# Kernel tuning notes

Hardware: AMD Instinct MI355X
Metric: run time of the kernel (lower is better)

## Reference

```python
import jax, jax.numpy as jnp
import numpy as np

B, E, H, SEQ = 4096, 512, 512, 128


def setup_inputs() -> dict:
    key = jax.random.key(0)
    ks = jax.random.split(key, 7)
    s = 1.0 / np.sqrt(H)  # PyTorch LSTM init scale
    return {
        "start_emb": jax.random.normal(ks[0], (B, 1, E), dtype=jnp.float32),
        "h0": jax.random.normal(ks[1], (1, B, H), dtype=jnp.float32),
        "c0": jax.random.normal(ks[2], (1, B, H), dtype=jnp.float32),
        "w_ih": jax.random.normal(ks[3], (4 * H, E), dtype=jnp.float32) * s,
        "w_hh": jax.random.normal(ks[4], (4 * H, H), dtype=jnp.float32) * s,
        "b_ih": jax.random.normal(ks[5], (4 * H,), dtype=jnp.float32) * s,
        "b_hh": jax.random.normal(ks[6], (4 * H,), dtype=jnp.float32) * s,
        "seq_length": SEQ,
    }


def reference(start_emb, h0, c0, w_ih, w_hh, b_ih, b_hh, seq_length):
    # start_emb: [B, 1, E] -- identical input every step, so precompute its projection once.
    x = start_emb[:, 0, :]                       # [B, E]
    x_proj = x @ w_ih.T + b_ih + b_hh            # [B, 4H], constant across steps
    hdim = w_hh.shape[1]

    def step(carry, _):
        h, c = carry                              # each [B, H]
        gates = x_proj + h @ w_hh.T               # [B, 4H]
        i, f, g, o = jnp.split(gates, 4, axis=-1) # PyTorch gate order i,f,g,o
        i = jax.nn.sigmoid(i)
        f = jax.nn.sigmoid(f)
        g = jnp.tanh(g)
        o = jax.nn.sigmoid(o)
        c = f * c + i * g
        h = o * jnp.tanh(c)
        return (h, c), None

    (h, c), _ = jax.lax.scan(step, (h0[0], c0[0]), None, length=seq_length)
    # Return final (h_n, c_n) with the [num_layers=1, B, H] leading dim, as PyTorch does.
    return h[None], c[None]
```

## Files before the change

### kernel.cpp

```cpp
#include <hip/hip_runtime.h>
#include <hip/hip_bf16.h>

#define BATCH 4096
#define KD    512
#define NG    2048
#define SEQLEN 128

typedef __attribute__((ext_vector_type(8))) short short8;
typedef __attribute__((ext_vector_type(4))) float floatx4;

#define HWREG_XCC_ID (20 | (0 << 6) | ((4 - 1) << 11))

__device__ __forceinline__ void gld16(const void* g, void* l) {
  __builtin_amdgcn_global_load_lds(
      (const __attribute__((address_space(1))) void*)g,
      (__attribute__((address_space(3))) void*)l, 16, 0, 0);
}

__device__ __forceinline__ float fast_sig(float x) {
  return __builtin_amdgcn_rcpf(1.0f + __expf(-x));
}
__device__ __forceinline__ float fast_tanh(float x) {
  return 1.0f - 2.0f * __builtin_amdgcn_rcpf(1.0f + __expf(2.0f * x));
}

__device__ __forceinline__ unsigned pack_bf16(float lo, float hi) {
  unsigned ul = (unsigned)__builtin_bit_cast(unsigned short, __float2bfloat16(lo));
  unsigned uh = (unsigned)__builtin_bit_cast(unsigned short, __float2bfloat16(hi));
  return (uh << 16) | ul;
}
__device__ __forceinline__ float unpack_lo(unsigned u) {
  u <<= 16; return __builtin_bit_cast(float, u);
}
__device__ __forceinline__ float unpack_hi(unsigned u) {
  u &= 0xffff0000u; return __builtin_bit_cast(float, u);
}

template <int TBM, int TBN, int NT>
__device__ __forceinline__ void gemm_tile(const short* __restrict__ A,
                                          const short* __restrict__ Bw,
                                          floatx4 acc[4][4],
                                          short* lA, short* lB,
                                          int bm, int bn,
                                          int lane, int wm, int wn, int tid) {
#pragma unroll 1
  for (int kt = 0; kt < KD / 64; ++kt) {
    const int k0 = kt * 64;
#pragma unroll
    for (int i = 0; i < TBM * 8 / NT; ++i) {
      int q = i * NT + tid;
      int row = q >> 3, cs = q & 7;
      int cc = cs ^ (row & 7);
      gld16(A + (size_t)(bm + row) * KD + k0 + cc * 8, lA + q * 8);
    }
#pragma unroll
    for (int i = 0; i < TBN * 8 / NT; ++i) {
      int q = i * NT + tid;
      int row = q >> 3, cs = q & 7;
      int cc = cs ^ (row & 7);
      gld16(Bw + (size_t)(bn + row) * KD + k0 + cc * 8, lB + q * 8);
    }
    __syncthreads();
#pragma unroll
    for (int ks = 0; ks < 2; ++ks) {
      short8 a[4], b[4];
#pragma unroll
      for (int mi = 0; mi < 4; ++mi) {
        int arow = wm * 64 + mi * 16 + (lane & 15);
        int ch = (ks * 4 + (lane >> 4)) ^ (arow & 7);
        a[mi] = *(const short8*)&lA[arow * 64 + ch * 8];
      }
#pragma unroll
      for (int j = 0; j < 4; ++j) {
        int brow = wn * 64 + j * 16 + (lane & 15);
        int ch = (ks * 4 + (lane >> 4)) ^ (brow & 7);
        b[j] = *(const short8*)&lB[brow * 64 + ch * 8];
      }
#pragma unroll
      for (int mi = 0; mi < 4; ++mi)
#pragma unroll
        for (int j = 0; j < 4; ++j)
          acc[mi][j] =
              __builtin_amdgcn_mfma_f32_16x16x32_bf16(a[mi], b[j], acc[mi][j], 0, 0, 0);
    }
    __syncthreads();
  }
}

__device__ __forceinline__ void group_barrier_xcd(unsigned* cnt, unsigned target) {
  __syncthreads();
  if (threadIdx.x == 0) {
    __hip_atomic_fetch_add(cnt, 1u, __ATOMIC_RELAXED, __HIP_MEMORY_SCOPE_AGENT);
    while (__hip_atomic_load(cnt, __ATOMIC_RELAXED, __HIP_MEMORY_SCOPE_AGENT) <
           target) {
      __builtin_amdgcn_s_sleep(1);
    }
    asm volatile("buffer_inv sc0" ::: "memory");
    asm volatile("s_waitcnt vmcnt(0)" ::: "memory");
  }
  __syncthreads();
}

__global__ __launch_bounds__(256, 2) void lstm_persist(
    const short* __restrict__ xbf,
    const short* __restrict__ wih,
    const short* __restrict__ whh,
    const float* __restrict__ biasp,
    const float* __restrict__ c0,
    short* __restrict__ hA, short* __restrict__ hB,
    float* __restrict__ outH, float* __restrict__ outC,
    unsigned* __restrict__ sync_area) {
  __shared__ __align__(16) short lA[128 * 64];
  __shared__ __align__(16) short lB[128 * 64 + 14336];

  const int tid = threadIdx.x;
  const int lane = tid & 63;
  const int wid = tid >> 6;
  const int wm = wid >> 1;
  const int wn = wid & 1;

  __shared__ int sh_bx, sh_by;
  if (tid == 0) {
    int px = __builtin_amdgcn_s_getreg(HWREG_XCC_ID) & 7;
    unsigned r = __hip_atomic_fetch_add(&sync_area[px], 1u, __ATOMIC_RELAXED,
                                        __HIP_MEMORY_SCOPE_AGENT);
    sh_bx = px * 4 + (int)((r >> 4) & 3);
    sh_by = (int)(r & 15);
  }
  __syncthreads();
  const int bx = sh_bx, by = sh_by;
  const int bm = bx * 128;
  const int bn = by * 128;
  unsigned* gcnt = sync_area + 256 + bx * 32;

  const int houter = by * 2 + wn;
  const int hcol = houter * 16 + (lane & 15);
  const int rb = houter * 64 + (lane & 15);

  floatx4 acc[4][4] = {};
  gemm_tile<128, 128, 256>(xbf, wih, acc, lA, lB, bm, bn, lane, wm, wn, tid);

  const float b0 = biasp[rb], b1 = biasp[rb + 16], b2 = biasp[rb + 32],
              b3 = biasp[rb + 48];
  unsigned xprP[4][4][2];
  float creg[4][4];
#pragma unroll
  for (int mi = 0; mi < 4; ++mi) {
    const int mrow0 = bm + wm * 64 + mi * 16 + (lane >> 4) * 4;
#pragma unroll
    for (int reg = 0; reg < 4; ++reg) {
      xprP[mi][reg][0] = pack_bf16(acc[mi][0][reg] + b0, acc[mi][1][reg] + b1);
      xprP[mi][reg][1] = pack_bf16(acc[mi][2][reg] + b2, acc[mi][3][reg] + b3);
      creg[mi][reg] = c0[(size_t)(mrow0 + reg) * KD + hcol];
    }
  }

#pragma unroll 1
  for (int t = 0; t < SEQLEN; ++t) {
    const short* hin = (t & 1) ? hB : hA;
    short* hout = (t & 1) ? hA : hB;

#pragma unroll
    for (int mi = 0; mi < 4; ++mi)
#pragma unroll
      for (int j = 0; j < 4; ++j)
        acc[mi][j] = floatx4{0.f, 0.f, 0.f, 0.f};

    gemm_tile<128, 128, 256>(hin, whh, acc, lA, lB, bm, bn, lane, wm, wn, tid);

#pragma unroll
    for (int mi = 0; mi < 4; ++mi) {
      const int mrow0 = bm + wm * 64 + mi * 16 + (lane >> 4) * 4;
#pragma unroll
      for (int reg = 0; reg < 4; ++reg) {
        const int m = mrow0 + reg;
        float gi = acc[mi][0][reg] + unpack_lo(xprP[mi][reg][0]);
        float gf = acc[mi][1][reg] + unpack_hi(xprP[mi][reg][0]);
        float gg = acc[mi][2][reg] + unpack_lo(xprP[mi][reg][1]);
        float go = acc[mi][3][reg] + unpack_hi(xprP[mi][reg][1]);
        float si = fast_sig(gi);
        float sf = fast_sig(gf);
        float tg = fast_tanh(gg);
        float so = fast_sig(go);
        float cn = sf * creg[mi][reg] + si * tg;
        creg[mi][reg] = cn;
        float hn = so * fast_tanh(cn);
        const size_t ci = (size_t)m * KD + hcol;
        ((__hip_bfloat16*)hout)[ci] = __float2bfloat16(hn);
        if (t == SEQLEN - 1) {
          outH[ci] = hn;
          outC[ci] = cn;
        }
      }
    }
    if (t != SEQLEN - 1) group_barrier_xcd(gcnt, 16u * (unsigned)(t + 1));
  }
}

__global__ __launch_bounds__(256, 2) void lstm_step(
    const short* __restrict__ hin, __hip_bfloat16* __restrict__ hout_bf,
    const short* __restrict__ W, const float* __restrict__ xp,
    float* __restrict__ c, float* __restrict__ hout_f32) {
  __shared__ __align__(16) short lA[128 * 64];
  __shared__ __align__(16) short lB[128 * 64];
  const int tid = threadIdx.x;
  const int lane = tid & 63;
  const int wid = tid >> 6;
  const int wm = wid >> 1, wn = wid & 1;
  const int bm = blockIdx.x * 128, bn = blockIdx.y * 128;

  floatx4 acc[4][4] = {};
  gemm_tile<128, 128, 256>(hin, W, acc, lA, lB, bm, bn, lane, wm, wn, tid);

  const int houter = blockIdx.y * 2 + wn;
  const int hcol = houter * 16 + (lane & 15);
  const int rb = houter * 64 + (lane & 15);
#pragma unroll
  for (int mi = 0; mi < 4; ++mi) {
    const int mrow0 = bm + wm * 64 + mi * 16 + (lane >> 4) * 4;
#pragma unroll
    for (int reg = 0; reg < 4; ++reg) {
      const int m = mrow0 + reg;
      const float* xpr = xp + (size_t)m * NG + rb;
      float si = fast_sig(acc[mi][0][reg] + xpr[0]);
      float sf = fast_sig(acc[mi][1][reg] + xpr[16]);
      float tg = fast_tanh(acc[mi][2][reg] + xpr[32]);
      float so = fast_sig(acc[mi][3][reg] + xpr[48]);
      const int ci = m * KD + hcol;
      float cn = sf * c[ci] + si * tg;
      c[ci] = cn;
      float hn = so * fast_tanh(cn);
      hout_bf[ci] = __float2bfloat16(hn);
      if (hout_f32) hout_f32[ci] = hn;
    }
  }
}

__global__ __launch_bounds__(256, 2) void xproj_gemm(
    const short* __restrict__ xbf, const short* __restrict__ Wih,
    const float* __restrict__ biasp, float* __restrict__ xp) {
  __shared__ __align__(16) short lA[128 * 64];
  __shared__ __align__(16) short lB[128 * 64];
  const int tid = threadIdx.x;
  const int lane = tid & 63;
  const int wid = tid >> 6;
  const int wm = wid >> 1, wn = wid & 1;
  const int bm = blockIdx.x * 128, bn = blockIdx.y * 128;

  floatx4 acc[4][4] = {};
  gemm_tile<128, 128, 256>(xbf, Wih, acc, lA, lB, bm, bn, lane, wm, wn, tid);

  const int houter = blockIdx.y * 2 + wn;
  const int rb = houter * 64 + (lane & 15);
  const float b0 = biasp[rb], b1 = biasp[rb + 16], b2 = biasp[rb + 32],
              b3 = biasp[rb + 48];
#pragma unroll
  for (int mi = 0; mi < 4; ++mi) {
    const int mrow0 = bm + wm * 64 + mi * 16 + (lane >> 4) * 4;
#pragma unroll
    for (int reg = 0; reg < 4; ++reg) {
      float* xpr = xp + (size_t)(mrow0 + reg) * NG + rb;
      xpr[0]  = acc[mi][0][reg] + b0;
      xpr[16] = acc[mi][1][reg] + b1;
      xpr[32] = acc[mi][2][reg] + b2;
      xpr[48] = acc[mi][3][reg] + b3;
    }
  }
}

__global__ void permw_k(const float* __restrict__ w,
                        __hip_bfloat16* __restrict__ o) {
  int idx = blockIdx.x * 256 + threadIdx.x;
  int r = idx >> 9, k = idx & 511;
  int hout = r >> 6, g = (r >> 4) & 3, hin = r & 15;
  o[idx] = __float2bfloat16(w[(size_t)((g << 9) + hout * 16 + hin) * 512 + k]);
}

__global__ void bias_k(const float* __restrict__ bi, const float* __restrict__ bh,
                       float* __restrict__ o) {
  int r = blockIdx.x * 256 + threadIdx.x;
  int hout = r >> 6, g = (r >> 4) & 3, hin = r & 15;
  int n = (g << 9) + hout * 16 + hin;
  o[r] = bi[n] + bh[n];
}

__global__ void f2bf_k(const float* __restrict__ in,
                       __hip_bfloat16* __restrict__ out, int n) {
  int i = blockIdx.x * 256 + threadIdx.x;
  if (i < n) out[i] = __float2bfloat16(in[i]);
}

extern "C" void kernel_launch(void* const* d_in, const int* in_sizes, int n_in,
                              void* d_out, int out_size, void* d_ws, size_t ws_size,
                              hipStream_t stream) {
  const float* start_emb = (const float*)d_in[0];
  const float* h0 = (const float*)d_in[1];
  const float* c0 = (const float*)d_in[2];
  const float* w_ih = (const float*)d_in[3];
  const float* w_hh = (const float*)d_in[4];
  const float* b_ih = (const float*)d_in[5];
  const float* b_hh = (const float*)d_in[6];

  char* ws = (char*)d_ws;
  __hip_bfloat16* whh_p = (__hip_bfloat16*)(ws);
  __hip_bfloat16* wih_p = (__hip_bfloat16*)(ws + (2ll << 20));
  __hip_bfloat16* xbf   = (__hip_bfloat16*)(ws + (4ll << 20));
  __hip_bfloat16* hbufA = (__hip_bfloat16*)(ws + (8ll << 20));
  __hip_bfloat16* hbufB = (__hip_bfloat16*)(ws + (12ll << 20));
  float* biasp          = (float*)(ws + (16ll << 20));
  unsigned* sync_area   = (unsigned*)(ws + (16ll << 20) + 65536);
  float* xp             = (float*)(ws + (17ll << 20));

  float* outH = (float*)d_out;
  float* outC = (float*)d_out + (size_t)BATCH * KD;

  permw_k<<<4096, 256, 0, stream>>>(w_hh, whh_p);
  permw_k<<<4096, 256, 0, stream>>>(w_ih, wih_p);
  bias_k<<<8, 256, 0, stream>>>(b_ih, b_hh, biasp);
  f2bf_k<<<8192, 256, 0, stream>>>(start_emb, xbf, BATCH * KD);
  f2bf_k<<<8192, 256, 0, stream>>>(h0, hbufA, BATCH * KD);
  (void)hipMemsetAsync(sync_area, 0, 8192, stream);

  const short* a_xbf = (const short*)xbf;
  const short* a_wih = (const short*)wih_p;
  const short* a_whh = (const short*)whh_p;
  const float* a_bias = biasp;
  const float* a_c0 = c0;
  short* a_hA = (short*)hbufA;
  short* a_hB = (short*)hbufB;
  float* a_outH = outH;
  float* a_outC = outC;
  unsigned* a_sync = sync_area;
  void* args[] = {&a_xbf, &a_wih, &a_whh, &a_bias, &a_c0,
                  &a_hA, &a_hB, &a_outH, &a_outC, &a_sync};
  hipError_t e = hipLaunchCooperativeKernel((const void*)lstm_persist,
                                            dim3(512), dim3(256), args,
                                            0, stream);
  if (e != hipSuccess) {
    (void)hipMemcpyAsync(outC, c0, (size_t)BATCH * KD * sizeof(float),
                         hipMemcpyDeviceToDevice, stream);
    dim3 grid(BATCH / 128, NG / 128);
    xproj_gemm<<<grid, 256, 0, stream>>>((const short*)xbf, (const short*)wih_p,
                                         biasp, xp);
    for (int t = 0; t < SEQLEN; ++t) {
      const short* hin = (const short*)((t & 1) ? hbufB : hbufA);
      __hip_bfloat16* hout = (t & 1) ? hbufA : hbufB;
      lstm_step<<<grid, 256, 0, stream>>>(hin, hout, (const short*)whh_p, xp,
                                          outC, (t == SEQLEN - 1) ? outH : nullptr);
    }
  }
}
```

Measured before the change: 1.696 ms.

## Keep the recurrent weight panel resident in LDS across all LSTM timesteps

The persistent LSTM kernel now loads each block's 128-row slice of W_ih, and then W_hh, once into a 128 KB LDS panel. It then streams only the h tiles at every step, instead of re-fetching weight tiles from L2/HBM each timestep. To fit this, blocks grow to 512 threads, each covering 256 batch rows, and the grid shrinks from 512 to 256 blocks with one block per CU. The inner K loop uses 32-wide steps with a new swizzle. A bounded spin counter was added to the group barrier so it cannot hang forever. The trade-offs are lower occupancy, more barriers per step, and high LDS pressure.

```diff
diff --git a/kernel.cpp b/kernel.cpp
--- a/kernel.cpp
+++ b/kernel.cpp
@@ -34,6 +34,61 @@
 }
 __device__ __forceinline__ float unpack_hi(unsigned u) {
   u &= 0xffff0000u; return __builtin_bit_cast(float, u);
+}
+
+__device__ __forceinline__ void load_panel(const short* __restrict__ W, int bn,
+                                           short* __restrict__ lWB, int tid) {
+#pragma unroll
+  for (int i = 0; i < 16; ++i) {
+    int q = i * 512 + tid;
+    int row = q >> 6, c = q & 63;
+    int c0 = (c & 56) | ((c & 7) ^ (row & 7));
+    gld16(W + (size_t)(bn + row) * KD + c0 * 8, lWB + q * 8);
+  }
+}
+
+__device__ __forceinline__ void gemm_panel(const short* __restrict__ A,
+                                           const short* __restrict__ lWB,
+                                           short* __restrict__ lA,
+                                           floatx4 acc[4][4],
+                                           int bm, int lane, int wm, int wn,
+                                           int tid) {
+#pragma unroll 1
+  for (int ht = 0; ht < 16; ++ht) {
+    const int k0 = ht * 32;
+#pragma unroll
+    for (int i = 0; i < 2; ++i) {
+      int q = i * 512 + tid;
+      int lr = q >> 3, c1 = q & 7;
+      int c0 = c1 ^ (lr & 7);
+      int row = lr * 2 + (c0 >> 2);
+      int kc = c0 & 3;
+      gld16(A + (size_t)(bm + row) * KD + k0 + kc * 8, lA + q * 8);
+    }
+    __syncthreads();
+    short8 a[4], b[4];
+#pragma unroll
+    for (int mi = 0; mi < 4; ++mi) {
+      int arow = wm * 64 + mi * 16 + (lane & 15);
+      int lr = arow >> 1;
+      int cc = (((arow & 1) << 2) + (lane >> 4)) ^ (lr & 7);
+      a[mi] = *(const short8*)&lA[lr * 64 + cc * 8];
+    }
+#pragma unroll
+    for (int j = 0; j < 4; ++j) {
+      int brow = wn * 64 + j * 16 + (lane & 15);
+      int c = ht * 4 + (lane >> 4);
+      int cc = (c & 56) | ((c & 7) ^ (brow & 7));
+      b[j] = *(const short8*)&lWB[brow * 512 + cc * 8];
+    }
+#pragma unroll
+    for (int mi = 0; mi < 4; ++mi)
+#pragma unroll
+      for (int j = 0; j < 4; ++j)
+        acc[mi][j] =
+            __builtin_amdgcn_mfma_f32_16x16x32_bf16(a[mi], b[j], acc[mi][j], 0, 0, 0);
+    __syncthreads();
+  }
 }
 
 template <int TBM, int TBN, int NT>
@@ -91,8 +146,10 @@
   __syncthreads();
   if (threadIdx.x == 0) {
     __hip_atomic_fetch_add(cnt, 1u, __ATOMIC_RELAXED, __HIP_MEMORY_SCOPE_AGENT);
+    unsigned guard = 0;
     while (__hip_atomic_load(cnt, __ATOMIC_RELAXED, __HIP_MEMORY_SCOPE_AGENT) <
-           target) {
+               target &&
+           ++guard < (1u << 20)) {
       __builtin_amdgcn_s_sleep(1);
     }
     asm volatile("buffer_inv sc0" ::: "memory");
@@ -101,7 +158,7 @@
   __syncthreads();
 }
 
-__global__ __launch_bounds__(256, 2) void lstm_persist(
+__global__ __launch_bounds__(512, 1) void lstm_persist(
     const short* __restrict__ xbf,
     const short* __restrict__ wih,
     const short* __restrict__ whh,
@@ -110,8 +167,9 @@
     short* __restrict__ hA, short* __restrict__ hB,
     float* __restrict__ outH, float* __restrict__ outC,
     unsigned* __restrict__ sync_area) {
+  __shared__ __align__(16) short lWB[128 * 512];
   __shared__ __align__(16) short lA[128 * 64];
-  __shared__ __align__(16) short lB[128 * 64 + 14336];
+  __shared__ int sh_gid, sh_by;
 
   const int tid = threadIdx.x;
   const int lane = tid & 63;
@@ -119,26 +177,27 @@
   const int wm = wid >> 1;
   const int wn = wid & 1;
 
-  __shared__ int sh_bx, sh_by;
   if (tid == 0) {
     int px = __builtin_amdgcn_s_getreg(HWREG_XCC_ID) & 7;
     unsigned r = __hip_atomic_fetch_add(&sync_area[px], 1u, __ATOMIC_RELAXED,
                                         __HIP_MEMORY_SCOPE_AGENT);
-    sh_bx = px * 4 + (int)((r >> 4) & 3);
+    sh_gid = px * 2 + (int)((r >> 4) & 1);
     sh_by = (int)(r & 15);
   }
   __syncthreads();
-  const int bx = sh_bx, by = sh_by;
-  const int bm = bx * 128;
+  const int gid = sh_gid, by = sh_by;
+  const int bm = gid * 256;
   const int bn = by * 128;
-  unsigned* gcnt = sync_area + 256 + bx * 32;
+  unsigned* gcnt = sync_area + 256 + gid * 32;
 
   const int houter = by * 2 + wn;
   const int hcol = houter * 16 + (lane & 15);
   const int rb = houter * 64 + (lane & 15);
 
+  load_panel(wih, bn, lWB, tid);
+  __syncthreads();
   floatx4 acc[4][4] = {};
-  gemm_tile<128, 128, 256>(xbf, wih, acc, lA, lB, bm, bn, lane, wm, wn, tid);
+  gemm_panel(xbf, lWB, lA, acc, bm, lane, wm, wn, tid);
 
   const float b0 = biasp[rb], b1 = biasp[rb + 16], b2 = biasp[rb + 32],
               b3 = biasp[rb + 48];
@@ -155,6 +214,9 @@
     }
   }
 
+  load_panel(whh, bn, lWB, tid);
+  __syncthreads();
+
 #pragma unroll 1
   for (int t = 0; t < SEQLEN; ++t) {
     const short* hin = (t & 1) ? hB : hA;
@@ -166,7 +228,7 @@
       for (int j = 0; j < 4; ++j)
         acc[mi][j] = floatx4{0.f, 0.f, 0.f, 0.f};
 
-    gemm_tile<128, 128, 256>(hin, whh, acc, lA, lB, bm, bn, lane, wm, wn, tid);
+    gemm_panel(hin, lWB, lA, acc, bm, lane, wm, wn, tid);
 
 #pragma unroll
     for (int mi = 0; mi < 4; ++mi) {
@@ -334,7 +396,7 @@
   void* args[] = {&a_xbf, &a_wih, &a_whh, &a_bias, &a_c0,
                   &a_hA, &a_hB, &a_outH, &a_outC, &a_sync};
   hipError_t e = hipLaunchCooperativeKernel((const void*)lstm_persist,
-                                            dim3(512), dim3(256), args,
+                                            dim3(256), dim3(512), args,
                                             0, stream);
   if (e != hipSuccess) {
     (void)hipMemcpyAsync(outC, c0, (size_t)BATCH * KD * sizeof(float),
```

After: 1.816 ms. +7.1%, slower.
